# Kernel tuning notes

Hardware: AMD Instinct MI355X
Metric: run time of the kernel (lower is better)

Reference implementation:

```python
import jax, jax.numpy as jnp
import numpy as np

N_SERIES = 100000
INPUT_SIZE = 28
OUTPUT_SIZE = 7
N_T = 1
N_S = 4
PERIOD = 7            # seasonality = [7]
EMBED = 1 + 1 + PERIOD  # lev_sms, seas_sms, init seasonal factors
BATCH = 2048
N_TIME = 2048


def setup_inputs() -> dict:
    key = jax.random.key(0)
    k1, k2, k3, k4 = jax.random.split(key, 4)
    # Y must be strictly positive (multiplicative model: division + log)
    Y = jax.random.uniform(k1, (BATCH, N_TIME), dtype=jnp.float32, minval=0.5, maxval=1.5)
    X = jax.random.normal(k2, (BATCH, N_T, N_TIME), dtype=jnp.float32)
    S = jax.random.normal(k3, (BATCH, N_S), dtype=jnp.float32)
    idxs = jax.random.randint(k4, (BATCH,), 0, N_SERIES)
    embeds_weight = jnp.full((N_SERIES, EMBED), 0.5, dtype=jnp.float32)
    return {"S": S, "Y": Y, "X": X, "idxs": idxs,
            "embeds_weight": embeds_weight, "step_size": 7}


def _levels_seasons(Y, idxs, embeds_weight):
    """Exponential smoothing level/seasonality recurrence (single seasonality)."""
    emb = embeds_weight[idxs]                      # (B, 9)
    lev_sms = jax.nn.sigmoid(emb[:, 0])            # (B,)
    seas_sms = jax.nn.sigmoid(emb[:, 1])           # (B,)
    init_seas = jnp.exp(emb[:, 2:2 + PERIOD])      # (B, 7)

    level0 = Y[:, 0] / init_seas[:, 0]
    # ring buffer holding the seasonal factors used at steps t=1..: [s1..s6, s0]
    buf0 = jnp.concatenate([init_seas[:, 1:], init_seas[:, :1]], axis=1)  # (B, 7)

    def step(carry, inp):
        lev, buf = carry
        y, k = inp
        s = jnp.take(buf, k % PERIOD, axis=1)                       # seasonality at lag PERIOD
        newlev = lev_sms * (y / s) + (1.0 - lev_sms) * lev
        news = seas_sms * (y / newlev) + (1.0 - seas_sms) * s
        buf = jax.lax.dynamic_update_slice_in_dim(buf, news[:, None], k % PERIOD, axis=1)
        return (newlev, buf), (newlev, news)

    ks = jnp.arange(N_TIME - 1, dtype=jnp.int32)
    (_, _), (levs, seas) = jax.lax.scan(step, (level0, buf0), (Y[:, 1:].T, ks))
    levels = jnp.concatenate([level0[:, None], levs.T], axis=1)           # (B, n_time)
    seasonal = jnp.concatenate([init_seas, init_seas[:, :1], seas.T], axis=1)  # (B, n_time+7)
    return levels, seasonal


def reference(S, Y, X, idxs, embeds_weight, step_size):
    levels, seasonal = _levels_seasons(Y, idxs, embeds_weight)

    windows_end = N_TIME - INPUT_SIZE - OUTPUT_SIZE + 1
    windows = np.arange(0, windows_end, step_size)          # static window starts
    W = len(windows)

    # --- insample windows, normalized: log(Y / level / season) ---
    idx_in = windows[:, None] + np.arange(INPUT_SIZE)       # (W, I)
    Yw = Y[:, idx_in]                                       # (B, W, I)
    lev_w = levels[:, windows + INPUT_SIZE - 1]             # (B, W)
    seas_w = seasonal[:, idx_in]                            # (B, W, I)
    y_in = jnp.log(Yw / (lev_w[:, :, None] * seas_w))
    y_in = y_in.transpose(1, 0, 2)                          # (W, B, I)

    # --- exogenous windows: X[:, :, start:start+I+O].reshape(B, -1) ---
    idx_x = windows[:, None] + np.arange(INPUT_SIZE + OUTPUT_SIZE)  # (W, I+O)
    Xw = X[:, :, idx_x].transpose(2, 0, 1, 3).reshape(W, BATCH, N_T * (INPUT_SIZE + OUTPUT_SIZE))

    # --- static features ---
    Sw = jnp.broadcast_to(S[None], (W, BATCH, N_S))

    windows_y_insample = jnp.concatenate([y_in, Xw, Sw], axis=2)   # (W, B, context)

    # --- outsample windows (eval mode: not normalized) ---
    idx_out = windows[:, None] + INPUT_SIZE + np.arange(OUTPUT_SIZE)  # (W, O)
    windows_y_outsample = Y[:, idx_out].transpose(1, 0, 2)            # (W, B, O)

    return windows_y_insample, windows_y_outsample, levels, seasonal
```

## Files before the change

### kernel.cpp

```cpp
#include <hip/hip_runtime.h>
#include <math.h>

#define BATCH 2048
#define N_TIME 2048
#define INPUT_SIZE 28
#define OUTPUT_SIZE 7
#define N_S 4
#define PERIOD 7
#define EMBED 9
#define SEAS_LEN (N_TIME + PERIOD)
#define W_COUNT 288
#define WB_COUNT (W_COUNT * BATCH)
#define INS_COLS 67
#define OUT0_SIZE (WB_COUNT * INS_COLS)
#define OUT1_SIZE (WB_COUNT * OUTPUT_SIZE)
#define LEV_SIZE (BATCH * N_TIME)
#define SEAS_SIZE (BATCH * SEAS_LEN)

struct ScanState {
    float lev, lev_sms, seas_sms, oma, oms;
    float buf[PERIOD];
};

template<bool PREF, bool LAST>
__device__ __forceinline__ void scan_chunk(
    int base, int l, int r0, int jr, int km,
    const float* __restrict__ Yb,
    float (&cur)[64], float (&nxt)[64],
    float (*__restrict__ tl)[65], float (*__restrict__ ts)[65],
    ScanState& st,
    float* __restrict__ levels, float* __restrict__ seasonal)
{
    if (PREF) {
#pragma unroll
        for (int k = 0; k < 64; k += 4)
            *(float4*)&nxt[k] = *(const float4*)(Yb + base + 64 + k);
    }
    tl[l][0] = st.lev;
#pragma unroll
    for (int k = 0; k < 64; ++k) {
        if (!LAST || k < 63) {
            float y  = (k < 63) ? cur[k + 1] : nxt[0];
            float s0 = st.buf[0];
            float nl = fmaf(st.oma, st.lev,
                            st.lev_sms * (y * __builtin_amdgcn_rcpf(s0)));
            float ns = fmaf(st.oms, s0,
                            st.seas_sms * (y * __builtin_amdgcn_rcpf(nl)));
#pragma unroll
            for (int q = 0; q < PERIOD - 1; ++q) st.buf[q] = st.buf[q + 1];
            st.buf[PERIOD - 1] = ns;
            st.lev = nl;
            tl[l][k + 1] = nl;
            ts[l][k]     = ns;
        }
    }
    __syncthreads();
#pragma unroll
    for (int j0 = 0; j0 < 64; j0 += 4) {
        int j = j0 + jr;
        float vl[4], vs[4];
#pragma unroll
        for (int i = 0; i < 4; ++i) { vl[i] = tl[j][km + i]; vs[i] = ts[j][km + i]; }
        float4 v4; v4.x = vl[0]; v4.y = vl[1]; v4.z = vl[2]; v4.w = vl[3];
        *(float4*)(levels + (size_t)(r0 + j) * N_TIME + base + km) = v4;
        float* srow = seasonal + (size_t)(r0 + j) * SEAS_LEN + base + 8 + km;
#pragma unroll
        for (int i = 0; i < 4; ++i)
            if (!LAST || (km + i) < 63) srow[i] = vs[i];
    }
    __syncthreads();
}

__global__ __launch_bounds__(64) void es_scan(
    const float* __restrict__ Y, const int* __restrict__ idxs,
    const float* __restrict__ emb,
    float* __restrict__ levels, float* __restrict__ seasonal)
{
    __shared__ float tl[64][65];
    __shared__ float ts[64][65];
    const int l  = threadIdx.x;
    const int r0 = blockIdx.x * 64;
    const int b  = r0 + l;
    const float* Yb = Y + (size_t)b * N_TIME;
    const int jr = l >> 4;
    const int km = (l & 15) * 4;

    const float* e = emb + (size_t)idxs[b] * EMBED;
    ScanState st;
    st.lev_sms  = 1.0f / (1.0f + __expf(-e[0]));
    st.seas_sms = 1.0f / (1.0f + __expf(-e[1]));
    st.oma = 1.0f - st.lev_sms;
    st.oms = 1.0f - st.seas_sms;
    float is[PERIOD];
#pragma unroll
    for (int j = 0; j < PERIOD; ++j) is[j] = __expf(e[2 + j]);
    st.lev = Yb[0] / is[0];

    float* seab = seasonal + (size_t)b * SEAS_LEN;
#pragma unroll
    for (int j = 0; j < PERIOD; ++j) seab[j] = is[j];
    seab[PERIOD] = is[0];
#pragma unroll
    for (int j = 0; j < PERIOD; ++j) st.buf[j] = is[(j + 1) % PERIOD];

    float ya[64], yb2[64];
#pragma unroll
    for (int k = 0; k < 64; k += 4)
        *(float4*)&ya[k] = *(const float4*)(Yb + k);

#pragma unroll 1
    for (int cc = 0; cc < 15; ++cc) {
        scan_chunk<true, false>(cc * 128,      l, r0, jr, km, Yb, ya, yb2, tl, ts, st, levels, seasonal);
        scan_chunk<true, false>(cc * 128 + 64, l, r0, jr, km, Yb, yb2, ya, tl, ts, st, levels, seasonal);
    }
    scan_chunk<true,  false>(1920, l, r0, jr, km, Yb, ya, yb2, tl, ts, st, levels, seasonal);
    scan_chunk<false, true >(1984, l, r0, jr, km, Yb, yb2, ya, tl, ts, st, levels, seasonal);
}

__global__ __launch_bounds__(256) void es_windows(
    const float* __restrict__ Y, const float* __restrict__ X,
    const float* __restrict__ S, const float* __restrict__ levels,
    const float* __restrict__ seasonal,
    float* __restrict__ out0, float* __restrict__ out1)
{
    int gid = blockIdx.x * 256 + threadIdx.x;
    if (gid < OUT0_SIZE) {
        unsigned u  = (unsigned)gid;
        unsigned wb = u / 67u;
        int j  = (int)(u - wb * 67u);
        int w  = (int)(wb >> 11);
        int b  = (int)(wb & (BATCH - 1));
        int t0 = w * 7;
        float v;
        if (j < INPUT_SIZE) {
            float y  = Y[b * N_TIME + t0 + j];
            float lv = levels[b * N_TIME + t0 + INPUT_SIZE - 1];
            float sv = seasonal[b * SEAS_LEN + t0 + j];
            v = __logf(y * __builtin_amdgcn_rcpf(lv * sv));
        } else if (j < 63) {
            v = X[b * N_TIME + t0 + (j - INPUT_SIZE)];
        } else {
            v = S[b * N_S + (j - 63)];
        }
        out0[gid] = v;
    } else {
        unsigned e  = (unsigned)(gid - OUT0_SIZE);
        unsigned wb = e / 7u;
        int m  = (int)(e - wb * 7u);
        int w  = (int)(wb >> 11);
        int b  = (int)(wb & (BATCH - 1));
        out1[e] = Y[b * N_TIME + w * 7 + INPUT_SIZE + m];
    }
}

extern "C" void kernel_launch(void* const* d_in, const int* in_sizes, int n_in,
                              void* d_out, int out_size, void* d_ws, size_t ws_size,
                              hipStream_t stream) {
    const float* S    = (const float*)d_in[0];
    const float* Y    = (const float*)d_in[1];
    const float* X    = (const float*)d_in[2];
    const int*   idxs = (const int*)d_in[3];
    const float* emb  = (const float*)d_in[4];

    float* out      = (float*)d_out;
    float* out_ins  = out;
    float* out_outs = out + OUT0_SIZE;
    float* levels   = out + OUT0_SIZE + OUT1_SIZE;
    float* seasonal = out + OUT0_SIZE + OUT1_SIZE + LEV_SIZE;

    es_scan<<<BATCH / 64, 64, 0, stream>>>(Y, idxs, emb, levels, seasonal);

    const int total = OUT0_SIZE + OUT1_SIZE;
    es_windows<<<total / 256, 256, 0, stream>>>(
        Y, X, S, levels, seasonal, out_ins, out_outs);
}
```

Measured before the change: 427.8 us.

## Shorten scan critical path by deferring seasonal update and precomputing reciprocals

```diff
diff --git a/kernel.cpp b/kernel.cpp
--- a/kernel.cpp
+++ b/kernel.cpp
@@ -18,11 +18,13 @@
 #define SEAS_SIZE (BATCH * SEAS_LEN)
 
 struct ScanState {
-    float lev, lev_sms, seas_sms, oma, oms;
-    float buf[PERIOD];
+    float lev, lsms, seas_sms, oma, oms;
+    float sbuf[PERIOD];
+    float rbuf[PERIOD];
+    float yp, sp, rnlp, rnsp;
 };
 
-template<bool PREF, bool LAST>
+template<bool FIRST, bool LAST, bool PREF>
 __device__ __forceinline__ void scan_chunk(
     int base, int l, int r0, int jr, int km,
     const float* __restrict__ Yb,
@@ -41,20 +43,33 @@
     for (int k = 0; k < 64; ++k) {
         if (!LAST || k < 63) {
             float y  = (k < 63) ? cur[k + 1] : nxt[0];
-            float s0 = st.buf[0];
-            float nl = fmaf(st.oma, st.lev,
-                            st.lev_sms * (y * __builtin_amdgcn_rcpf(s0)));
-            float ns = fmaf(st.oms, s0,
-                            st.seas_sms * (y * __builtin_amdgcn_rcpf(nl)));
-#pragma unroll
-            for (int q = 0; q < PERIOD - 1; ++q) st.buf[q] = st.buf[q + 1];
-            st.buf[PERIOD - 1] = ns;
+            float s0 = st.sbuf[0];
+            float nl = fmaf(st.oma, st.lev, y * st.rbuf[0]);
             st.lev = nl;
             tl[l][k + 1] = nl;
-            ts[l][k]     = ns;
+            if (!FIRST || k > 0) {
+                float u  = st.yp * st.rnlp;
+                float ns = fmaf(st.oms, st.sp, st.seas_sms * u);
+                ts[l][k] = ns;
+                st.sbuf[PERIOD - 1] = ns;
+                if (!FIRST || k > 1)
+                    st.rbuf[PERIOD - 2] = st.lsms * st.rnsp;
+                st.rnsp = __builtin_amdgcn_rcpf(ns);
+            }
+            float rnl = __builtin_amdgcn_rcpf(nl);
+#pragma unroll
+            for (int q = 0; q < PERIOD - 1; ++q) st.sbuf[q] = st.sbuf[q + 1];
+#pragma unroll
+            for (int q = 0; q < PERIOD - 1; ++q) st.rbuf[q] = st.rbuf[q + 1];
+            st.yp = y; st.sp = s0; st.rnlp = rnl;
         }
     }
-    __syncthreads();
+    if (LAST) {
+        float u  = st.yp * st.rnlp;
+        float ns = fmaf(st.oms, st.sp, st.seas_sms * u);
+        ts[l][63] = ns;
+    }
+    asm volatile("s_waitcnt lgkmcnt(0)" ::: "memory");
 #pragma unroll
     for (int j0 = 0; j0 < 64; j0 += 4) {
         int j = j0 + jr;
@@ -63,12 +78,11 @@
         for (int i = 0; i < 4; ++i) { vl[i] = tl[j][km + i]; vs[i] = ts[j][km + i]; }
         float4 v4; v4.x = vl[0]; v4.y = vl[1]; v4.z = vl[2]; v4.w = vl[3];
         *(float4*)(levels + (size_t)(r0 + j) * N_TIME + base + km) = v4;
-        float* srow = seasonal + (size_t)(r0 + j) * SEAS_LEN + base + 8 + km;
+        float* srow = seasonal + (size_t)(r0 + j) * SEAS_LEN + base + 7 + km;
 #pragma unroll
-        for (int i = 0; i < 4; ++i)
-            if (!LAST || (km + i) < 63) srow[i] = vs[i];
+        for (int i = 0; i < 4; ++i) srow[i] = vs[i];
     }
-    __syncthreads();
+    asm volatile("s_waitcnt lgkmcnt(0)" ::: "memory");
 }
 
 __global__ __launch_bounds__(64) void es_scan(
@@ -87,9 +101,9 @@
 
     const float* e = emb + (size_t)idxs[b] * EMBED;
     ScanState st;
-    st.lev_sms  = 1.0f / (1.0f + __expf(-e[0]));
+    st.lsms     = 1.0f / (1.0f + __expf(-e[0]));
     st.seas_sms = 1.0f / (1.0f + __expf(-e[1]));
-    st.oma = 1.0f - st.lev_sms;
+    st.oma = 1.0f - st.lsms;
     st.oms = 1.0f - st.seas_sms;
     float is[PERIOD];
 #pragma unroll
@@ -99,22 +113,26 @@
     float* seab = seasonal + (size_t)b * SEAS_LEN;
 #pragma unroll
     for (int j = 0; j < PERIOD; ++j) seab[j] = is[j];
-    seab[PERIOD] = is[0];
+    ts[l][0] = is[0];
 #pragma unroll
-    for (int j = 0; j < PERIOD; ++j) st.buf[j] = is[(j + 1) % PERIOD];
+    for (int j = 0; j < PERIOD; ++j) st.sbuf[j] = is[(j + 1) % PERIOD];
+#pragma unroll
+    for (int j = 0; j < PERIOD; ++j)
+        st.rbuf[j] = st.lsms * __builtin_amdgcn_rcpf(st.sbuf[j]);
+    st.yp = 0.0f; st.sp = 1.0f; st.rnlp = 1.0f; st.rnsp = 1.0f;
 
     float ya[64], yb2[64];
 #pragma unroll
     for (int k = 0; k < 64; k += 4)
         *(float4*)&ya[k] = *(const float4*)(Yb + k);
 
+    scan_chunk<true,  false, true >(0, l, r0, jr, km, Yb, ya, yb2, tl, ts, st, levels, seasonal);
 #pragma unroll 1
     for (int cc = 0; cc < 15; ++cc) {
-        scan_chunk<true, false>(cc * 128,      l, r0, jr, km, Yb, ya, yb2, tl, ts, st, levels, seasonal);
-        scan_chunk<true, false>(cc * 128 + 64, l, r0, jr, km, Yb, yb2, ya, tl, ts, st, levels, seasonal);
+        scan_chunk<false, false, true>(64  + cc * 128, l, r0, jr, km, Yb, yb2, ya, tl, ts, st, levels, seasonal);
+        scan_chunk<false, false, true>(128 + cc * 128, l, r0, jr, km, Yb, ya, yb2, tl, ts, st, levels, seasonal);
     }
-    scan_chunk<true,  false>(1920, l, r0, jr, km, Yb, ya, yb2, tl, ts, st, levels, seasonal);
-    scan_chunk<false, true >(1984, l, r0, jr, km, Yb, yb2, ya, tl, ts, st, levels, seasonal);
+    scan_chunk<false, true,  false>(1984, l, r0, jr, km, Yb, yb2, ya, tl, ts, st, levels, seasonal);
 }
 
 __global__ __launch_bounds__(256) void es_windows(
```

Result: faster. 414.6 us (-3.1%).
